# Performance work log

Hardware: AMD Instinct MI355X
Metric: run time of the kernel (lower is better)

## Reference

```python
import jax, jax.numpy as jnp
import numpy as np

B, S, D, H, HD = 2, 4096, 768, 12, 64
W = 256  # one-sided attention window (attention_window=512 // 2)
SCALE = 1.0 / np.sqrt(HD).astype(np.float32)
NEG = -1e9


def setup_inputs() -> dict:
    key = jax.random.key(0)
    ks = jax.random.split(key, 13)
    inp = {"hidden_states": jax.random.normal(ks[0], (B, S, D), dtype=jnp.float32)}
    names = ["Wq", "Wk", "Wv", "Wqg", "Wkg", "Wvg"]
    for i, n in enumerate(names):
        inp[n] = jax.random.normal(ks[1 + i], (D, D), dtype=jnp.float32) * 0.02
        inp["b" + n[1:]] = jax.random.normal(ks[7 + i], (D,), dtype=jnp.float32) * 0.02
    inp["num_global"] = 32
    return inp


def _heads(x):
    # [B,S,D] -> [B,H,S,HD]
    return x.reshape(B, S, H, HD).transpose(0, 2, 1, 3)


def longformer_attn(hidden_states, Wq, bq, Wk, bk, Wv, bv, Wqg, bqg, Wkg, bkg, Wvg, bvg, G):
    q = _heads(hidden_states @ Wq + bq) * SCALE
    k = _heads(hidden_states @ Wk + bk)
    v = _heads(hidden_states @ Wv + bv)

    nc = S // W  # number of query chunks
    # --- banded (sliding window) scores via overlapping key chunks of size 3W ---
    Qc = q.reshape(B, H, nc, W, HD)
    kpad = jnp.pad(k, ((0, 0), (0, 0), (W, W), (0, 0)))
    win_idx = jnp.arange(nc)[:, None] * W + jnp.arange(3 * W)[None, :]  # [nc, 3W]
    K3 = kpad[:, :, win_idx]  # [B,H,nc,3W,HD]
    band = jnp.einsum('bhcqd,bhckd->bhcqk', Qc, K3)  # [B,H,nc,W,3W]
    # mask: key abs position in range, and relative offset within [-W, W]
    c = jnp.arange(nc)[:, None, None]
    pq = jnp.arange(W)[None, :, None]
    e = jnp.arange(3 * W)[None, None, :]
    kabs = c * W + e - W
    valid = (kabs >= 0) & (kabs < S) & (e >= pq) & (e <= pq + 2 * W)
    band = jnp.where(valid[None, None], band, NEG).reshape(B, H, S, 3 * W)

    # --- all queries also attend to the G global keys (regular key proj) ---
    sg = jnp.einsum('bhsd,bhgd->bhsg', q, k[:, :, :G])  # [B,H,S,G]
    probs = jax.nn.softmax(jnp.concatenate([sg, band], axis=-1), axis=-1)
    pg, pb = probs[..., :G], probs[..., G:].reshape(B, H, nc, W, 3 * W)

    vpad = jnp.pad(v, ((0, 0), (0, 0), (W, W), (0, 0)))
    V3 = vpad[:, :, win_idx]  # [B,H,nc,3W,HD]
    out = jnp.einsum('bhcqk,bhckd->bhcqd', pb, V3).reshape(B, H, S, HD)
    out = out + jnp.einsum('bhsg,bhgd->bhsd', pg, v[:, :, :G])

    # --- global queries attend to ALL tokens with the *_global projections ---
    qg = _heads(hidden_states @ Wqg + bqg)[:, :, :G] * SCALE  # [B,H,G,HD]
    kgf = _heads(hidden_states @ Wkg + bkg)
    vgf = _heads(hidden_states @ Wvg + bvg)
    gp = jax.nn.softmax(jnp.einsum('bhgd,bhsd->bhgs', qg, kgf), axis=-1)
    gout = jnp.einsum('bhgs,bhsd->bhgd', gp, vgf)  # [B,H,G,HD]
    out = out.at[:, :, :G].set(gout)

    return out.transpose(0, 2, 1, 3).reshape(B, S, D)


def reference(hidden_states, Wq, bq, Wk, bk, Wv, bv, Wqg, bqg, Wkg, bkg, Wvg, bvg, num_global):
    return longformer_attn(hidden_states, Wq, bq, Wk, bk, Wv, bv, Wqg, bqg, Wkg, bkg, Wvg, bvg, int(num_global))
```

## Files before the change

### kernel.cpp

```cpp
#include <hip/hip_runtime.h>
#include <hip/hip_bf16.h>


#define DEVI __device__ __forceinline__
typedef _Float16 f16;
typedef _Float16 h4 __attribute__((ext_vector_type(4)));
typedef _Float16 f16x8 __attribute__((ext_vector_type(8)));
typedef __attribute__((ext_vector_type(4))) float float4v;

DEVI float4v mfma16(f16x8 a, f16x8 b, float4v c) {
    return __builtin_amdgcn_mfma_f32_16x16x32_f16(a, b, c, 0, 0, 0);
}

DEVI void gl_lds16(const f16* g, f16* l) {
    __builtin_amdgcn_global_load_lds(
        (const __attribute__((address_space(1))) unsigned int*)g,
        (__attribute__((address_space(3))) unsigned int*)l, 16, 0, 0);
}

__global__ __launch_bounds__(256) void prep(
    const float* __restrict__ x,
    const float* __restrict__ w0, const float* __restrict__ w1,
    const float* __restrict__ w2, const float* __restrict__ w3,
    const float* __restrict__ w4, const float* __restrict__ w5,
    f16* __restrict__ xh, f16* __restrict__ wt) {
    __shared__ float tile[64][65];
    int bid = blockIdx.x;
    if (bid < 6144) {
        int i = (bid * 256 + threadIdx.x) * 4;
        float4 v = *(const float4*)&x[i];
        h4 o = {(f16)v.x, (f16)v.y, (f16)v.z, (f16)v.w};
        *(h4*)&xh[i] = o;
    } else {
        int t = bid - 6144;
        int i = t / 144, rem = t - i * 144;
        int n0 = (rem % 12) * 64, k0 = (rem / 12) * 64;
        const float* W = (i == 0) ? w0 : (i == 1) ? w1 : (i == 2) ? w2
                       : (i == 3) ? w3 : (i == 4) ? w4 : w5;
        int tx = threadIdx.x & 63, ty = threadIdx.x >> 6;
#pragma unroll
        for (int yy = 0; yy < 64; yy += 4)
            tile[yy + ty][tx] = W[(size_t)(k0 + yy + ty) * 768 + n0 + tx];
        __syncthreads();
#pragma unroll
        for (int yy = 0; yy < 64; yy += 4)
            wt[(size_t)(i * 768 + n0 + yy + ty) * 768 + k0 + tx] = (f16)tile[tx][yy + ty];
    }
}

__global__ __launch_bounds__(256) void qkv_mfma5(
    const f16* __restrict__ Xh, const f16* __restrict__ Wt,
    const float* __restrict__ b0, const float* __restrict__ b1,
    const float* __restrict__ b2, const float* __restrict__ b3,
    const float* __restrict__ b4, const float* __restrict__ b5,
    f16* __restrict__ q, f16* __restrict__ k, f16* __restrict__ vT,
    f16* __restrict__ qg, f16* __restrict__ kg, f16* __restrict__ vgT) {
    constexpr int CLD = 136;
    __shared__ __align__(16) char smem[128 * CLD * 2];
    f16* At0 = (f16*)smem;
    f16* Bt0 = (f16*)(smem + 8192);
    f16* At1 = (f16*)(smem + 16384);
    f16* Bt1 = (f16*)(smem + 24576);
    f16* Cl = (f16*)smem;
    int tid = threadIdx.x, lane = tid & 63, wid = tid >> 6;
    int quad = lane >> 4, l15 = lane & 15;
    int m0 = blockIdx.x * 128;
    int grp = blockIdx.y / 6;
    if (grp == 3 && (m0 & 4095) != 0) return;
    int wm = (wid >> 1) * 64, wn = (wid & 1) * 64;
    const f16* arow0 = Xh + (size_t)m0 * 768;
    const f16* brow0 = Wt + (size_t)blockIdx.y * 128 * 768;

    float4v acc[4][4];
#pragma unroll
    for (int mt = 0; mt < 4; ++mt)
#pragma unroll
        for (int nt = 0; nt < 4; ++nt) acc[mt][nt] = (float4v){0.f, 0.f, 0.f, 0.f};

    int s0 = tid, s1 = tid + 256;
    int r0 = s0 >> 2, r1 = s1 >> 2;
    int o0 = (((s0 & 3) ^ ((r0 >> 1) & 3)) << 3);
    int o1 = (((s1 & 3) ^ ((r1 >> 1) & 3)) << 3);
    int sw8 = ((quad ^ ((l15 >> 1) & 3)) << 3);

    auto STAGE = [&](int kt, f16* A, f16* B) {
        int k0 = kt << 5;
        gl_lds16(&arow0[(size_t)r0 * 768 + k0 + o0], A + wid * 512);
        gl_lds16(&brow0[(size_t)r0 * 768 + k0 + o0], B + wid * 512);
        gl_lds16(&arow0[(size_t)r1 * 768 + k0 + o1], A + 2048 + wid * 512);
        gl_lds16(&brow0[(size_t)r1 * 768 + k0 + o1], B + 2048 + wid * 512);
    };

    f16* Ac = At0; f16* Bc = Bt0; f16* An = At1; f16* Bn = Bt1;
    STAGE(0, Ac, Bc);
    __syncthreads();
    for (int kt = 0; kt < 24; ++kt) {
        if (kt < 23) STAGE(kt + 1, An, Bn);
        f16x8 af[4], bf[4];
#pragma unroll
        for (int mt = 0; mt < 4; ++mt)
            af[mt] = *(const f16x8*)&Ac[(wm + mt * 16 + l15) * 32 + sw8];
#pragma unroll
        for (int nt = 0; nt < 4; ++nt)
            bf[nt] = *(const f16x8*)&Bc[(wn + nt * 16 + l15) * 32 + sw8];
#pragma unroll
        for (int mt = 0; mt < 4; ++mt)
#pragma unroll
            for (int nt = 0; nt < 4; ++nt) acc[mt][nt] = mfma16(af[mt], bf[nt], acc[mt][nt]);
        __syncthreads();
        f16* t;
        t = Ac; Ac = An; An = t;
        t = Bc; Bc = Bn; Bn = t;
    }

    const float* Bsel = (grp == 0) ? b0 : (grp == 1) ? b1 : (grp == 2) ? b2
                      : (grp == 3) ? b3 : (grp == 4) ? b4 : b5;
    int nb = (blockIdx.y - grp * 6) * 128;
    int b = m0 >> 12;
    bool tr = (grp == 2 || grp == 5);

    if (tr) {
#pragma unroll
        for (int nt = 0; nt < 4; ++nt) {
            float bias = Bsel[nb + wn + nt * 16 + l15];
#pragma unroll
            for (int mt = 0; mt < 4; ++mt) {
                float4v a = acc[mt][nt];
                h4 pk = {(f16)(a[0] + bias), (f16)(a[1] + bias),
                         (f16)(a[2] + bias), (f16)(a[3] + bias)};
                *(h4*)&Cl[(wn + nt * 16 + l15) * CLD + wm + mt * 16 + quad * 4] = pk;
            }
        }
    } else {
        float scale = (grp == 0 || grp == 3) ? 0.125f : 1.0f;
#pragma unroll
        for (int nt = 0; nt < 4; ++nt) {
            float bias = Bsel[nb + wn + nt * 16 + l15];
#pragma unroll
            for (int mt = 0; mt < 4; ++mt) {
                float4v a = acc[mt][nt];
#pragma unroll
                for (int r = 0; r < 4; ++r)
                    Cl[(wm + mt * 16 + quad * 4 + r) * CLD + wn + nt * 16 + l15] =
                        (f16)((a[r] + bias) * scale);
            }
        }
    }
    __syncthreads();

    if (tr) {
        f16* base = (grp == 2) ? vT : vgT;
        int c = tid & 127, sh = (tid >> 7) * 64;
        int ncol = nb + c, h = ncol >> 6, hd = ncol & 63;
        f16* dst = &base[((size_t)((b * 12 + h) * 64 + hd)) * 4096 + (m0 & 4095) + sh];
        const f16* src = &Cl[c * CLD + sh];
#pragma unroll
        for (int i = 0; i < 8; ++i)
            *(f16x8*)&dst[i * 8] = *(const f16x8*)&src[i * 8];
    } else {
        int sl = tid & 127, hh = tid >> 7;
        int s = (m0 & 4095) + sl;
        int h = (nb + hh * 64) >> 6;
        const f16* src = &Cl[sl * CLD + hh * 64];
        f16* dst = nullptr;
        if (grp == 3) {
            if (s < 32) dst = &qg[((size_t)((b * 12 + h) * 32 + s)) * 64];
        } else {
            f16* baseb = (grp == 0) ? q : (grp == 1) ? k : kg;
            dst = &baseb[((size_t)((b * 12 + h) * 4096 + s)) * 64];
        }
        if (dst)
#pragma unroll
            for (int i = 0; i < 8; ++i)
                *(f16x8*)&dst[i * 8] = *(const f16x8*)&src[i * 8];
    }
}

__global__ __launch_bounds__(256, 3) void band_mfma5(
    const f16* __restrict__ q, const f16* __restrict__ k, const f16* __restrict__ vT,
    float* __restrict__ out) {
    constexpr int LDK = 72, LDV = 136, LDP = 40;
    __shared__ __align__(16) f16 Kt[128 * LDK];
    __shared__ __align__(16) f16 Vt[64 * LDV];
    __shared__ __align__(16) f16 Pt[4][32 * LDP];
    int tid = threadIdx.x, lane = tid & 63, wid = tid >> 6;
    int quad = lane >> 4, l15 = lane & 15;
    int c = blockIdx.x & 31, h = (blockIdx.x >> 5) % 12, b = blockIdx.x / 384;
    const f16* qsl = q + (size_t)(b * 12 + h) * 4096 * 64;
    const f16* ksl = k + (size_t)(b * 12 + h) * 4096 * 64;
    const f16* vsl = vT + (size_t)(b * 12 + h) * 64 * 4096;
    int q0 = c * 128;
    int pq0 = q0 + wid * 32;

    f16x8 qf[2][2];
#pragma unroll
    for (int qg = 0; qg < 2; ++qg)
#pragma unroll
        for (int ks = 0; ks < 2; ++ks)
            qf[qg][ks] = *(const f16x8*)&qsl[(size_t)(pq0 + qg * 16 + l15) * 64 +
                                             ks * 32 + quad * 8];

    float4v Ot[4][2];
#pragma unroll
    for (int dt = 0; dt < 4; ++dt)
#pragma unroll
        for (int qg = 0; qg < 2; ++qg) Ot[dt][qg] = (float4v){0.f, 0.f, 0.f, 0.f};
    float lacc[2] = {0.f, 0.f};
    f16* PW = &Pt[wid][0];

    {
#pragma unroll
        for (int jt = 0; jt < 2; ++jt) {
            f16x8 kf0 = *(const f16x8*)&ksl[(size_t)(jt * 16 + l15) * 64 + quad * 8];
            f16x8 kf1 = *(const f16x8*)&ksl[(size_t)(jt * 16 + l15) * 64 + 32 + quad * 8];
#pragma unroll
            for (int qg = 0; qg < 2; ++qg) {
                float4v sacc = (float4v){0.f, 0.f, 0.f, 0.f};
                sacc = mfma16(kf0, qf[qg][0], sacc);
                sacc = mfma16(kf1, qf[qg][1], sacc);
                float p0 = __expf(sacc[0]), p1 = __expf(sacc[1]);
                float p2 = __expf(sacc[2]), p3 = __expf(sacc[3]);
                lacc[qg] += (p0 + p1) + (p2 + p3);
                h4 pk = {(f16)p0, (f16)p1, (f16)p2, (f16)p3};
                *(h4*)&PW[(qg * 16 + l15) * LDP + jt * 16 + quad * 4] = pk;
            }
        }
        f16x8 pf0 = *(const f16x8*)&PW[l15 * LDP + quad * 8];
        f16x8 pf1 = *(const f16x8*)&PW[(16 + l15) * LDP + quad * 8];
#pragma unroll
        for (int dt = 0; dt < 4; ++dt) {
            f16x8 vf = *(const f16x8*)&vsl[(size_t)(dt * 16 + l15) * 4096 + quad * 8];
            Ot[dt][0] = mfma16(vf, pf0, Ot[dt][0]);
            Ot[dt][1] = mfma16(vf, pf1, Ot[dt][1]);
        }
    }

    for (int r = 0; r < 5; ++r) {
        int kb = q0 - 256 + r * 128;
        if (kb < 0 || kb >= 4096) continue;
        __syncthreads();
        {
            int kr = tid >> 1, ko = (tid & 1) * 32;
            const f16* ks2 = &ksl[(size_t)(kb + kr) * 64 + ko];
            f16* kd = &Kt[kr * LDK + ko];
#pragma unroll
            for (int i = 0; i < 4; ++i) *(f16x8*)&kd[i * 8] = *(const f16x8*)&ks2[i * 8];
            int vr = tid >> 2, vo = (tid & 3) * 32;
            const f16* vs2 = &vsl[(size_t)vr * 4096 + kb + vo];
            f16* vd = &Vt[vr * LDV + vo];
#pragma unroll
            for (int i = 0; i < 4; ++i) *(f16x8*)&vd[i * 8] = *(const f16x8*)&vs2[i * 8];
        }
        __syncthreads();

        if (kb + 127 < pq0 - 256 || kb > pq0 + 287) continue;

#pragma unroll
        for (int tt = 0; tt < 2; ++tt) {
            int tb = kb + tt * 64;
            if (tb + 63 < pq0 - 256 || tb > pq0 + 287) continue;
#pragma unroll
            for (int hf = 0; hf < 2; ++hf) {
#pragma unroll
                for (int jt = 0; jt < 2; ++jt) {
                    int jl = tt * 64 + hf * 32 + jt * 16;
                    f16x8 kf0 = *(const f16x8*)&Kt[(jl + l15) * LDK + quad * 8];
                    f16x8 kf1 = *(const f16x8*)&Kt[(jl + l15) * LDK + 32 + quad * 8];
                    int j0 = kb + jl;
#pragma unroll
                    for (int qg = 0; qg < 2; ++qg) {
                        int qlo = pq0 + qg * 16;
                        h4 pk = {(f16)0.f, (f16)0.f, (f16)0.f, (f16)0.f};
                        bool dead = (j0 < qlo - 271) || (j0 > qlo + 271);
                        if (!dead) {
                            float4v sacc = (float4v){0.f, 0.f, 0.f, 0.f};
                            sacc = mfma16(kf0, qf[qg][0], sacc);
                            sacc = mfma16(kf1, qf[qg][1], sacc);
                            float p[4];
                            bool full = (j0 >= qlo - 241) && (j0 <= qlo + 241);
                            if (full) {
#pragma unroll
                                for (int rr = 0; rr < 4; ++rr) p[rr] = __expf(sacc[rr]);
                            } else {
#pragma unroll
                                for (int rr = 0; rr < 4; ++rr) {
                                    int d = (j0 + quad * 4 + rr) - (qlo + l15);
                                    p[rr] = ((unsigned)(d + 256) <= 512u) ? __expf(sacc[rr]) : 0.f;
                                }
                            }
                            lacc[qg] += (p[0] + p[1]) + (p[2] + p[3]);
                            pk = (h4){(f16)p[0], (f16)p[1], (f16)p[2], (f16)p[3]};
                        }
                        *(h4*)&PW[(qg * 16 + l15) * LDP + jt * 16 + quad * 4] = pk;
                    }
                }
                f16x8 pf0 = *(const f16x8*)&PW[l15 * LDP + quad * 8];
                f16x8 pf1 = *(const f16x8*)&PW[(16 + l15) * LDP + quad * 8];
#pragma unroll
                for (int dt = 0; dt < 4; ++dt) {
                    f16x8 vf = *(const f16x8*)&Vt[(dt * 16 + l15) * LDV +
                                                  tt * 64 + hf * 32 + quad * 8];
                    Ot[dt][0] = mfma16(vf, pf0, Ot[dt][0]);
                    Ot[dt][1] = mfma16(vf, pf1, Ot[dt][1]);
                }
            }
        }
    }

#pragma unroll
    for (int qg = 0; qg < 2; ++qg) {
        float lsum = lacc[qg];
        lsum += __shfl_xor(lsum, 16);
        lsum += __shfl_xor(lsum, 32);
        float inv = 1.f / lsum;
        size_t orow = (size_t)(b * 4096 + pq0 + qg * 16 + l15) * 768 + h * 64;
#pragma unroll
        for (int dt = 0; dt < 4; ++dt) {
            float4 o4 = {Ot[dt][qg][0] * inv, Ot[dt][qg][1] * inv,
                         Ot[dt][qg][2] * inv, Ot[dt][qg][3] * inv};
            *(float4*)&out[orow + dt * 16 + quad * 4] = o4;
        }
    }
}

__global__ __launch_bounds__(256) void global_part(
    const f16* __restrict__ qg, const f16* __restrict__ kg, const f16* __restrict__ vgT,
    float* __restrict__ Opart, float* __restrict__ Lpart) {
    constexpr int LDP = 72;
    __shared__ __align__(16) f16 Pt[4][32 * LDP];
    __shared__ __align__(16) float Osh[4][64 * 32];
    __shared__ float Lsh[4][32];
    int tid = threadIdx.x, lane = tid & 63, wid = tid >> 6;
    int quad = lane >> 4, l15 = lane & 15;
    int sl = blockIdx.x & 7, bh = blockIdx.x >> 3;
    const f16* qsl = qg + (size_t)bh * 32 * 64;
    const f16* ksl = kg + (size_t)bh * 4096 * 64;
    const f16* vsl = vgT + (size_t)bh * 64 * 4096;
    int kbase = sl * 512 + wid * 128;

    f16x8 qf[2][2];
#pragma unroll
    for (int g = 0; g < 2; ++g)
#pragma unroll
        for (int ks = 0; ks < 2; ++ks)
            qf[g][ks] = *(const f16x8*)&qsl[(size_t)(g * 16 + l15) * 64 + ks * 32 + quad * 8];

    float4v Ot[4][2];
#pragma unroll
    for (int dt = 0; dt < 4; ++dt)
#pragma unroll
        for (int g = 0; g < 2; ++g) Ot[dt][g] = (float4v){0.f, 0.f, 0.f, 0.f};
    float lacc[2] = {0.f, 0.f};
    f16* PW = &Pt[wid][0];

#pragma unroll
    for (int hf = 0; hf < 2; ++hf) {
        int kh0 = kbase + hf * 64;
#pragma unroll
        for (int kt = 0; kt < 4; ++kt) {
            int jb = kh0 + kt * 16;
            f16x8 kf0 = *(const f16x8*)&ksl[(size_t)(jb + l15) * 64 + quad * 8];
            f16x8 kf1 = *(const f16x8*)&ksl[(size_t)(jb + l15) * 64 + 32 + quad * 8];
#pragma unroll
            for (int g = 0; g < 2; ++g) {
                float4v sacc = (float4v){0.f, 0.f, 0.f, 0.f};
                sacc = mfma16(kf0, qf[g][0], sacc);
                sacc = mfma16(kf1, qf[g][1], sacc);
                float p0 = __expf(sacc[0]), p1 = __expf(sacc[1]);
                float p2 = __expf(sacc[2]), p3 = __expf(sacc[3]);
                lacc[g] += (p0 + p1) + (p2 + p3);
                h4 pk = {(f16)p0, (f16)p1, (f16)p2, (f16)p3};
                *(h4*)&PW[(g * 16 + l15) * LDP + kt * 16 + quad * 4] = pk;
            }
        }
#pragma unroll
        for (int kh = 0; kh < 2; ++kh) {
            f16x8 pf0 = *(const f16x8*)&PW[l15 * LDP + kh * 32 + quad * 8];
            f16x8 pf1 = *(const f16x8*)&PW[(16 + l15) * LDP + kh * 32 + quad * 8];
#pragma unroll
            for (int dt = 0; dt < 4; ++dt) {
                f16x8 vf = *(const f16x8*)&vsl[(size_t)(dt * 16 + l15) * 4096 +
                                               kh0 + kh * 32 + quad * 8];
                Ot[dt][0] = mfma16(vf, pf0, Ot[dt][0]);
                Ot[dt][1] = mfma16(vf, pf1, Ot[dt][1]);
            }
        }
    }

#pragma unroll
    for (int g = 0; g < 2; ++g) {
        lacc[g] += __shfl_xor(lacc[g], 16);
        lacc[g] += __shfl_xor(lacc[g], 32);
    }
    if (quad == 0) { Lsh[wid][l15] = lacc[0]; Lsh[wid][16 + l15] = lacc[1]; }
#pragma unroll
    for (int dt = 0; dt < 4; ++dt)
#pragma unroll
        for (int g = 0; g < 2; ++g)
#pragma unroll
            for (int r = 0; r < 4; ++r)
                Osh[wid][(dt * 16 + quad * 4 + r) * 32 + g * 16 + l15] = Ot[dt][g][r];
    __syncthreads();
#pragma unroll
    for (int i = 0; i < 8; ++i) {
        int idx = tid + i * 256;
        int d = idx & 63, qq = idx >> 6;
        float v = Osh[0][d * 32 + qq] + Osh[1][d * 32 + qq] +
                  Osh[2][d * 32 + qq] + Osh[3][d * 32 + qq];
        Opart[(size_t)blockIdx.x * 2048 + idx] = v;
    }
    if (tid < 32)
        Lpart[blockIdx.x * 32 + tid] = Lsh[0][tid] + Lsh[1][tid] + Lsh[2][tid] + Lsh[3][tid];
}

__global__ __launch_bounds__(256) void global_reduce(
    const float* __restrict__ Opart, const float* __restrict__ Lpart,
    float* __restrict__ out) {
    __shared__ float Ls[32];
    int tid = threadIdx.x, bh = blockIdx.x;
    int b = bh / 12, h = bh % 12;
    if (tid < 32) {
        float s = 0.f;
#pragma unroll
        for (int sl = 0; sl < 8; ++sl) s += Lpart[(bh * 8 + sl) * 32 + tid];
        Ls[tid] = s;
    }
    __syncthreads();
#pragma unroll
    for (int i = 0; i < 8; ++i) {
        int idx = tid + i * 256;
        int d = idx & 63, qq = idx >> 6;
        float o = 0.f;
#pragma unroll
        for (int sl = 0; sl < 8; ++sl) o += Opart[(size_t)(bh * 8 + sl) * 2048 + idx];
        out[(size_t)(b * 4096 + qq) * 768 + h * 64 + d] = o / Ls[qq];
    }
}

extern "C" void kernel_launch(void* const* d_in, const int* in_sizes, int n_in,
                              void* d_out, int out_size, void* d_ws, size_t ws_size,
                              hipStream_t stream) {
    const float* hs = (const float*)d_in[0];
    float* outp = (float*)d_out;

    char* p = (char*)d_ws;
    const size_t SLAB = (size_t)2 * 12 * 4096 * 64 * sizeof(f16);
    f16* qb   = (f16*)(p + 0 * SLAB);
    f16* kb   = (f16*)(p + 1 * SLAB);
    f16* vtb  = (f16*)(p + 2 * SLAB);
    f16* kgb  = (f16*)(p + 3 * SLAB);
    f16* vgtb = (f16*)(p + 4 * SLAB);
    f16* qgb  = (f16*)(p + 5 * SLAB);
    char* p2  = p + 5 * SLAB + 196608;
    f16* xh   = (f16*)p2;
    f16* wt   = (f16*)(p2 + SLAB);
    char* p3  = p2 + SLAB + 7077888;
    float* Opart = (float*)p3;
    float* Lpart = (float*)(p3 + 1572864);

    prep<<<7008, 256, 0, stream>>>(
        hs,
        (const float*)d_in[1], (const float*)d_in[3], (const float*)d_in[5],
        (const float*)d_in[7], (const float*)d_in[9], (const float*)d_in[11],
        xh, wt);
    qkv_mfma5<<<dim3(64, 36), 256, 0, stream>>>(
        xh, wt,
        (const float*)d_in[2], (const float*)d_in[4], (const float*)d_in[6],
        (const float*)d_in[8], (const float*)d_in[10], (const float*)d_in[12],
        qb, kb, vtb, qgb, kgb, vgtb);
    band_mfma5<<<768, 256, 0, stream>>>(qb, kb, vtb, outp);
    global_part<<<192, 256, 0, stream>>>(qgb, kgb, vgtb, Opart, Lpart);
    global_reduce<<<24, 256, 0, stream>>>(Opart, Lpart, outp);
}
```

Baseline: 235.6 us.

## Deepen QKV GEMM pipeline to four LDS stages with explicit vmcnt waits

Replaces the double-buffered K loop of the QKV projection GEMM with a four-buffer ring. Loads run three tiles ahead, and partial s_waitcnt vmcnt counts gate each tile instead of a full __syncthreads per iteration. The goal is to hide global-to-LDS load latency behind the MFMA work. LDS use grows from about 34KB to 64KB per block, which may lower occupancy, and correctness now depends on the hand-counted vmcnt values.

```diff
diff --git a/kernel.cpp b/kernel.cpp
--- a/kernel.cpp
+++ b/kernel.cpp
@@ -48,7 +48,7 @@
     }
 }
 
-__global__ __launch_bounds__(256) void qkv_mfma5(
+__global__ __launch_bounds__(256) void qkv_mfma6(
     const f16* __restrict__ Xh, const f16* __restrict__ Wt,
     const float* __restrict__ b0, const float* __restrict__ b1,
     const float* __restrict__ b2, const float* __restrict__ b3,
@@ -56,11 +56,15 @@
     f16* __restrict__ q, f16* __restrict__ k, f16* __restrict__ vT,
     f16* __restrict__ qg, f16* __restrict__ kg, f16* __restrict__ vgT) {
     constexpr int CLD = 136;
-    __shared__ __align__(16) char smem[128 * CLD * 2];
-    f16* At0 = (f16*)smem;
-    f16* Bt0 = (f16*)(smem + 8192);
-    f16* At1 = (f16*)(smem + 16384);
-    f16* Bt1 = (f16*)(smem + 24576);
+    __shared__ __align__(16) char smem[65536];
+    f16* A0 = (f16*)(smem);
+    f16* B0 = (f16*)(smem + 8192);
+    f16* A1 = (f16*)(smem + 16384);
+    f16* B1 = (f16*)(smem + 24576);
+    f16* A2 = (f16*)(smem + 32768);
+    f16* B2 = (f16*)(smem + 40960);
+    f16* A3 = (f16*)(smem + 49152);
+    f16* B3 = (f16*)(smem + 57344);
     f16* Cl = (f16*)smem;
     int tid = threadIdx.x, lane = tid & 63, wid = tid >> 6;
     int quad = lane >> 4, l15 = lane & 15;
@@ -91,27 +95,38 @@
         gl_lds16(&brow0[(size_t)r1 * 768 + k0 + o1], B + 2048 + wid * 512);
     };
 
-    f16* Ac = At0; f16* Bc = Bt0; f16* An = At1; f16* Bn = Bt1;
-    STAGE(0, Ac, Bc);
+#define QKV_ITER(T, CUR, DOSTAGE, STG, WN)                                    \
+    do {                                                                      \
+        asm volatile("s_waitcnt vmcnt(" #WN ")" ::: "memory");                \
+        __builtin_amdgcn_s_barrier();                                         \
+        __builtin_amdgcn_sched_barrier(0);                                    \
+        if (DOSTAGE) STAGE((T) + 3, A##STG, B##STG);                          \
+        f16x8 af[4], bf[4];                                                   \
+        _Pragma("unroll") for (int mt = 0; mt < 4; ++mt)                      \
+            af[mt] = *(const f16x8*)&A##CUR[(wm + mt * 16 + l15) * 32 + sw8]; \
+        _Pragma("unroll") for (int nt = 0; nt < 4; ++nt)                      \
+            bf[nt] = *(const f16x8*)&B##CUR[(wn + nt * 16 + l15) * 32 + sw8]; \
+        _Pragma("unroll") for (int mt = 0; mt < 4; ++mt)                      \
+            _Pragma("unroll") for (int nt = 0; nt < 4; ++nt)                  \
+                acc[mt][nt] = mfma16(af[mt], bf[nt], acc[mt][nt]);            \
+    } while (0)
+
+    STAGE(0, A0, B0);
+    STAGE(1, A1, B1);
+    STAGE(2, A2, B2);
+    for (int m = 0; m < 5; ++m) {
+        int t0 = m * 4;
+        QKV_ITER(t0 + 0, 0, true, 3, 8);
+        QKV_ITER(t0 + 1, 1, true, 0, 8);
+        QKV_ITER(t0 + 2, 2, true, 1, 8);
+        QKV_ITER(t0 + 3, 3, true, 2, 8);
+    }
+    QKV_ITER(20, 0, true, 3, 8);
+    QKV_ITER(21, 1, false, 0, 8);
+    QKV_ITER(22, 2, false, 0, 4);
+    QKV_ITER(23, 3, false, 0, 0);
+#undef QKV_ITER
     __syncthreads();
-    for (int kt = 0; kt < 24; ++kt) {
-        if (kt < 23) STAGE(kt + 1, An, Bn);
-        f16x8 af[4], bf[4];
-#pragma unroll
-        for (int mt = 0; mt < 4; ++mt)
-            af[mt] = *(const f16x8*)&Ac[(wm + mt * 16 + l15) * 32 + sw8];
-#pragma unroll
-        for (int nt = 0; nt < 4; ++nt)
-            bf[nt] = *(const f16x8*)&Bc[(wn + nt * 16 + l15) * 32 + sw8];
-#pragma unroll
-        for (int mt = 0; mt < 4; ++mt)
-#pragma unroll
-            for (int nt = 0; nt < 4; ++nt) acc[mt][nt] = mfma16(af[mt], bf[nt], acc[mt][nt]);
-        __syncthreads();
-        f16* t;
-        t = Ac; Ac = An; An = t;
-        t = Bc; Bc = Bn; Bn = t;
-    }
 
     const float* Bsel = (grp == 0) ? b0 : (grp == 1) ? b1 : (grp == 2) ? b2
                       : (grp == 3) ? b3 : (grp == 4) ? b4 : b5;
@@ -463,7 +478,7 @@
         (const float*)d_in[1], (const float*)d_in[3], (const float*)d_in[5],
         (const float*)d_in[7], (const float*)d_in[9], (const float*)d_in[11],
         xh, wt);
-    qkv_mfma5<<<dim3(64, 36), 256, 0, stream>>>(
+    qkv_mfma6<<<dim3(64, 36), 256, 0, stream>>>(
         xh, wt,
         (const float*)d_in[2], (const float*)d_in[4], (const float*)d_in[6],
         (const float*)d_in[8], (const float*)d_in[10], (const float*)d_in[12],
```

After: 229.2 us. -2.7%, faster.

## Deepen QKV GEMM load pipeline and remap blocks for XCD locality

Applied to the files above, without the earlier changes.

Replaces the double-buffered QKV projection GEMM loop with a fully unrolled multi-stage pipeline: A tiles are prefetched three k-steps ahead in a 4-deep ring and B tiles five ahead in a 6-deep ring. Explicit vmcnt waits, barriers and MFMA priority raises replace the per-iteration syncthreads. Block indices are also remapped so that blocks sharing the same M rows land on the same XCD, to improve L2 reuse. This hides global-load latency behind MFMA work, at the cost of much larger LDS use (80KB), which may reduce occupancy.

```diff
diff --git a/kernel.cpp b/kernel.cpp
--- a/kernel.cpp
+++ b/kernel.cpp
@@ -48,7 +48,7 @@
     }
 }
 
-__global__ __launch_bounds__(256) void qkv_mfma5(
+__global__ __launch_bounds__(256) void qkv_mfma8(
     const f16* __restrict__ Xh, const f16* __restrict__ Wt,
     const float* __restrict__ b0, const float* __restrict__ b1,
     const float* __restrict__ b2, const float* __restrict__ b3,
@@ -56,26 +56,31 @@
     f16* __restrict__ q, f16* __restrict__ k, f16* __restrict__ vT,
     f16* __restrict__ qg, f16* __restrict__ kg, f16* __restrict__ vgT) {
     constexpr int CLD = 136;
-    __shared__ __align__(16) char smem[128 * CLD * 2];
-    f16* At0 = (f16*)smem;
-    f16* Bt0 = (f16*)(smem + 8192);
-    f16* At1 = (f16*)(smem + 16384);
-    f16* Bt1 = (f16*)(smem + 24576);
+    __shared__ __align__(16) char smem[81920];
+    f16* As = (f16*)smem;
+    f16* Bs = (f16*)(smem + 32768);
     f16* Cl = (f16*)smem;
+
     int tid = threadIdx.x, lane = tid & 63, wid = tid >> 6;
     int quad = lane >> 4, l15 = lane & 15;
-    int m0 = blockIdx.x * 128;
-    int grp = blockIdx.y / 6;
+
+    int L = blockIdx.x + (blockIdx.y << 6);
+    int xcd = L & 7, W = L >> 3;
+    int mt = xcd * 8 + (W & 7);
+    int yy = W >> 3;
+    int m0 = mt * 128;
+    int grp = yy / 6;
     if (grp == 3 && (m0 & 4095) != 0) return;
+    int nb = (yy - grp * 6) * 128;
     int wm = (wid >> 1) * 64, wn = (wid & 1) * 64;
     const f16* arow0 = Xh + (size_t)m0 * 768;
-    const f16* brow0 = Wt + (size_t)blockIdx.y * 128 * 768;
+    const f16* brow0 = Wt + (size_t)(grp * 768 + nb) * 768;
 
     float4v acc[4][4];
 #pragma unroll
-    for (int mt = 0; mt < 4; ++mt)
-#pragma unroll
-        for (int nt = 0; nt < 4; ++nt) acc[mt][nt] = (float4v){0.f, 0.f, 0.f, 0.f};
+    for (int mtt = 0; mtt < 4; ++mtt)
+#pragma unroll
+        for (int ntt = 0; ntt < 4; ++ntt) acc[mtt][ntt] = (float4v){0.f, 0.f, 0.f, 0.f};
 
     int s0 = tid, s1 = tid + 256;
     int r0 = s0 >> 2, r1 = s1 >> 2;
@@ -83,39 +88,54 @@
     int o1 = (((s1 & 3) ^ ((r1 >> 1) & 3)) << 3);
     int sw8 = ((quad ^ ((l15 >> 1) & 3)) << 3);
 
-    auto STAGE = [&](int kt, f16* A, f16* B) {
+    auto STAGE_A = [&](int kt, int buf) {
         int k0 = kt << 5;
-        gl_lds16(&arow0[(size_t)r0 * 768 + k0 + o0], A + wid * 512);
-        gl_lds16(&brow0[(size_t)r0 * 768 + k0 + o0], B + wid * 512);
-        gl_lds16(&arow0[(size_t)r1 * 768 + k0 + o1], A + 2048 + wid * 512);
-        gl_lds16(&brow0[(size_t)r1 * 768 + k0 + o1], B + 2048 + wid * 512);
+        gl_lds16(&arow0[(size_t)r0 * 768 + k0 + o0], As + buf * 4096 + wid * 512);
+        gl_lds16(&arow0[(size_t)r1 * 768 + k0 + o1], As + buf * 4096 + 2048 + wid * 512);
     };
-
-    f16* Ac = At0; f16* Bc = Bt0; f16* An = At1; f16* Bn = Bt1;
-    STAGE(0, Ac, Bc);
+    auto STAGE_B = [&](int kt, int buf) {
+        int k0 = kt << 5;
+        gl_lds16(&brow0[(size_t)r0 * 768 + k0 + o0], Bs + buf * 4096 + wid * 512);
+        gl_lds16(&brow0[(size_t)r1 * 768 + k0 + o1], Bs + buf * 4096 + 2048 + wid * 512);
+    };
+
+#define QTILE(T, WN)                                                          \
+    do {                                                                      \
+        asm volatile("s_waitcnt vmcnt(" #WN ")" ::: "memory");                \
+        __builtin_amdgcn_s_barrier();                                         \
+        __builtin_amdgcn_sched_barrier(0);                                    \
+        if ((T) + 3 <= 23) STAGE_A((T) + 3, ((T) + 3) & 3);                   \
+        if ((T) + 5 <= 23) STAGE_B((T) + 5, ((T) + 5) % 6);                   \
+        const f16* Ab = As + ((T) & 3) * 4096;                                \
+        const f16* Bb = Bs + ((T) % 6) * 4096;                                \
+        f16x8 af[4], bf[4];                                                   \
+        _Pragma("unroll") for (int i = 0; i < 4; ++i)                         \
+            af[i] = *(const f16x8*)&Ab[(wm + i * 16 + l15) * 32 + sw8];       \
+        _Pragma("unroll") for (int j = 0; j < 4; ++j)                         \
+            bf[j] = *(const f16x8*)&Bb[(wn + j * 16 + l15) * 32 + sw8];       \
+        __builtin_amdgcn_s_setprio(1);                                        \
+        _Pragma("unroll") for (int i = 0; i < 4; ++i)                         \
+            _Pragma("unroll") for (int j = 0; j < 4; ++j)                     \
+                acc[i][j] = mfma16(af[i], bf[j], acc[i][j]);                  \
+        __builtin_amdgcn_s_setprio(0);                                        \
+    } while (0)
+
+    STAGE_A(0, 0); STAGE_A(1, 1); STAGE_A(2, 2);
+    STAGE_B(0, 0); STAGE_B(1, 1); STAGE_B(2, 2); STAGE_B(3, 3); STAGE_B(4, 4);
+    QTILE(0, 8);
+    QTILE(1, 10);  QTILE(2, 10);  QTILE(3, 10);  QTILE(4, 10);  QTILE(5, 10);
+    QTILE(6, 10);  QTILE(7, 10);  QTILE(8, 10);  QTILE(9, 10);  QTILE(10, 10);
+    QTILE(11, 10); QTILE(12, 10); QTILE(13, 10); QTILE(14, 10); QTILE(15, 10);
+    QTILE(16, 10); QTILE(17, 10); QTILE(18, 10); QTILE(19, 10);
+    QTILE(20, 8);
+    QTILE(21, 6);
+    QTILE(22, 2);
+    QTILE(23, 0);
+#undef QTILE
     __syncthreads();
-    for (int kt = 0; kt < 24; ++kt) {
-        if (kt < 23) STAGE(kt + 1, An, Bn);
-        f16x8 af[4], bf[4];
-#pragma unroll
-        for (int mt = 0; mt < 4; ++mt)
-            af[mt] = *(const f16x8*)&Ac[(wm + mt * 16 + l15) * 32 + sw8];
-#pragma unroll
-        for (int nt = 0; nt < 4; ++nt)
-            bf[nt] = *(const f16x8*)&Bc[(wn + nt * 16 + l15) * 32 + sw8];
-#pragma unroll
-        for (int mt = 0; mt < 4; ++mt)
-#pragma unroll
-            for (int nt = 0; nt < 4; ++nt) acc[mt][nt] = mfma16(af[mt], bf[nt], acc[mt][nt]);
-        __syncthreads();
-        f16* t;
-        t = Ac; Ac = An; An = t;
-        t = Bc; Bc = Bn; Bn = t;
-    }
 
     const float* Bsel = (grp == 0) ? b0 : (grp == 1) ? b1 : (grp == 2) ? b2
                       : (grp == 3) ? b3 : (grp == 4) ? b4 : b5;
-    int nb = (blockIdx.y - grp * 6) * 128;
     int b = m0 >> 12;
     bool tr = (grp == 2 || grp == 5);
 
@@ -124,11 +144,11 @@
         for (int nt = 0; nt < 4; ++nt) {
             float bias = Bsel[nb + wn + nt * 16 + l15];
 #pragma unroll
-            for (int mt = 0; mt < 4; ++mt) {
-                float4v a = acc[mt][nt];
+            for (int mtt = 0; mtt < 4; ++mtt) {
+                float4v a = acc[mtt][nt];
                 h4 pk = {(f16)(a[0] + bias), (f16)(a[1] + bias),
                          (f16)(a[2] + bias), (f16)(a[3] + bias)};
-                *(h4*)&Cl[(wn + nt * 16 + l15) * CLD + wm + mt * 16 + quad * 4] = pk;
+                *(h4*)&Cl[(wn + nt * 16 + l15) * CLD + wm + mtt * 16 + quad * 4] = pk;
             }
         }
     } else {
@@ -137,11 +157,11 @@
         for (int nt = 0; nt < 4; ++nt) {
             float bias = Bsel[nb + wn + nt * 16 + l15];
 #pragma unroll
-            for (int mt = 0; mt < 4; ++mt) {
-                float4v a = acc[mt][nt];
+            for (int mtt = 0; mtt < 4; ++mtt) {
+                float4v a = acc[mtt][nt];
 #pragma unroll
                 for (int r = 0; r < 4; ++r)
-                    Cl[(wm + mt * 16 + quad * 4 + r) * CLD + wn + nt * 16 + l15] =
+                    Cl[(wm + mtt * 16 + quad * 4 + r) * CLD + wn + nt * 16 + l15] =
                         (f16)((a[r] + bias) * scale);
             }
         }
@@ -463,7 +483,7 @@
         (const float*)d_in[1], (const float*)d_in[3], (const float*)d_in[5],
         (const float*)d_in[7], (const float*)d_in[9], (const float*)d_in[11],
         xh, wt);
-    qkv_mfma5<<<dim3(64, 36), 256, 0, stream>>>(
+    qkv_mfma8<<<dim3(64, 36), 256, 0, stream>>>(
         xh, wt,
         (const float*)d_in[2], (const float*)d_in[4], (const float*)d_in[6],
         (const float*)d_in[8], (const float*)d_in[10], (const float*)d_in[12],
```

Result: faster. 225.0 us (-4.5%).
